# Performance work log

Measured on AMD Instinct MI355X. Metric: run time of the kernel, lower is better.

Reference implementation:

```python
import jax, jax.numpy as jnp
import numpy as np
import math

B, S, D, M, H = 4, 2048, 1024, 512, 8
DK = M // H


def setup_inputs() -> dict:
    key = jax.random.key(0)
    ks = jax.random.split(key, 16)
    sd = lambda fan_in: 1.0 / math.sqrt(fan_in)
    inp = {
        'x': jax.random.normal(ks[0], (B, S, D), dtype=jnp.float32),
        'W_enc': jax.random.normal(ks[1], (D, M), dtype=jnp.float32) * sd(D),
        'b_enc': jnp.zeros((M,), jnp.float32),
        'Wq': jax.random.normal(ks[2], (M, M), dtype=jnp.float32) * sd(M),
        'bq': jnp.zeros((M,), jnp.float32),
        'Wk': jax.random.normal(ks[3], (M, M), dtype=jnp.float32) * sd(M),
        'bk': jnp.zeros((M,), jnp.float32),
        'Wv': jax.random.normal(ks[4], (M, M), dtype=jnp.float32) * sd(M),
        'bv': jnp.zeros((M,), jnp.float32),
        'Wo': jax.random.normal(ks[5], (M, M), dtype=jnp.float32) * sd(M),
        'bo': jnp.zeros((M,), jnp.float32),
        'ocr_bias': jnp.zeros((1, H, 1, 1), jnp.float32),  # learned, init zeros
        'W1': jax.random.normal(ks[6], (D + M, D), dtype=jnp.float32) * sd(D + M),
        'b1': jnp.zeros((D,), jnp.float32),
        'W2': jax.random.normal(ks[7], (D, D), dtype=jnp.float32) * sd(D),
        'b2': jnp.zeros((D,), jnp.float32),
        'ln_g': jnp.ones((D,), jnp.float32),
        'ln_b': jnp.zeros((D,), jnp.float32),
    }
    return inp


def _ocr_attention(m, Wq, bq, Wk, bk, Wv, bv, Wo, bo, ocr_bias):
    b, s, _ = m.shape
    q = (m @ Wq + bq).reshape(b, s, H, DK).transpose(0, 2, 1, 3)  # bhsd
    k = (m @ Wk + bk).reshape(b, s, H, DK).transpose(0, 2, 1, 3)
    v = (m @ Wv + bv).reshape(b, s, H, DK).transpose(0, 2, 1, 3)
    scores = jnp.einsum('bhqd,bhkd->bhqk', q, k) / math.sqrt(DK) + ocr_bias
    attn = jax.nn.softmax(scores, axis=-1)  # dropout is identity at eval
    ctx = jnp.einsum('bhqk,bhkd->bhqd', attn, v)
    ctx = ctx.transpose(0, 2, 1, 3).reshape(b, s, M)
    return ctx @ Wo + bo


def _layernorm(h, g, bta, eps=1e-5):
    mu = jnp.mean(h, axis=-1, keepdims=True)
    var = jnp.mean(jnp.square(h - mu), axis=-1, keepdims=True)
    return (h - mu) * jax.lax.rsqrt(var + eps) * g + bta


def reference(x, W_enc, b_enc, Wq, bq, Wk, bk, Wv, bv, Wo, bo, ocr_bias, W1, b1, W2, b2, ln_g, ln_b):
    mem = x @ W_enc + b_enc  # [B,S,M] memory-dim stream
    attended = _ocr_attention(mem, Wq, bq, Wk, bk, Wv, bv, Wo, bo, ocr_bias)
    h = jnp.concatenate([x, attended], axis=-1) @ W1 + b1  # [B,S,D]
    h = jax.nn.gelu(h, approximate=False)
    h = h @ W2 + b2
    return _layernorm(h, ln_g, ln_b)
```

## Files before the change

### kernel.cpp

```cpp
#include <hip/hip_runtime.h>
#include <math.h>

#define B_ 4
#define S_ 2048
#define D_ 1024
#define M_ 512
#define H_ 8
#define R_ (B_ * S_)

typedef __bf16 bf8_t __attribute__((ext_vector_type(8)));
typedef __bf16 bf4_t __attribute__((ext_vector_type(4)));
typedef float f4_t __attribute__((ext_vector_type(4)));

typedef __attribute__((address_space(3))) void lds_void;
typedef const __attribute__((address_space(1))) void gl_void;
#define GL16(gp, lp) __builtin_amdgcn_global_load_lds((gl_void*)(gp), (lds_void*)(lp), 16, 0, 0)

__device__ inline unsigned packbf2(float a, float b) {
  union { __bf16 h[2]; unsigned u; } c;
  c.h[0] = (__bf16)a;
  c.h[1] = (__bf16)b;
  return c.u;
}
__device__ inline unsigned bperm(int srcBytes, unsigned v) {
  return (unsigned)__builtin_amdgcn_ds_bpermute(srcBytes, (int)v);
}

struct PrepArgs {
  const float* src[7];
  __bf16* dst[7];
  int K[7], N[7];
  int start[8];
  const float* x;
  __bf16* ab;
};

__global__ __launch_bounds__(256) void k_prep(PrepArgs a) {
  const int t = threadIdx.x;
  const int id = blockIdx.x;
  if (id < a.start[7]) {
    int w = 0;
    while (id >= a.start[w + 1]) ++w;
    const int local = id - a.start[w];
    const int bxw = a.N[w] >> 5;
    const int n0 = (local % bxw) * 32;
    const int k0 = (local / bxw) * 32;
    const int tx = t & 31, ty = t >> 5;
    __shared__ float tile[32][33];
    const float* in = a.src[w];
    __bf16* out = a.dst[w];
    const int N = a.N[w], K = a.K[w];
#pragma unroll
    for (int j = 0; j < 32; j += 8)
      tile[ty + j][tx] = in[(size_t)(k0 + ty + j) * N + n0 + tx];
    __syncthreads();
#pragma unroll
    for (int j = 0; j < 32; j += 8)
      out[(size_t)(n0 + ty + j) * K + k0 + tx] = (__bf16)tile[tx][ty + j];
  } else {
    size_t i = (((size_t)(id - a.start[7])) * 256 + t) * 8;
    size_t row = i >> 10;
    size_t col = i & 1023;
    f4_t f0 = *(const f4_t*)(a.x + i);
    f4_t f1 = *(const f4_t*)(a.x + i + 4);
    bf8_t v;
    v[0] = (__bf16)f0[0]; v[1] = (__bf16)f0[1]; v[2] = (__bf16)f0[2]; v[3] = (__bf16)f0[3];
    v[4] = (__bf16)f1[0]; v[5] = (__bf16)f1[1]; v[6] = (__bf16)f1[2]; v[7] = (__bf16)f1[3];
    *(bf8_t*)(a.ab + row * 1536 + col) = v;
  }
}

template <int EPI>
__global__ __launch_bounds__(256) void k_gemm_bt(const __bf16* __restrict__ A, int lda,
                                                 const __bf16* __restrict__ Bt,
                                                 const float* __restrict__ bias,
                                                 __bf16* __restrict__ C, int ldc, int K) {
  __shared__ __bf16 As[128 * 32];
  __shared__ __bf16 Bs[128 * 32];
  const int t = threadIdx.x;
  const int lane = t & 63;
  const int wv = t >> 6;
  const int wr = (wv >> 1) * 64;
  const int wc = (wv & 1) * 64;
  const int bm = blockIdx.y * 128;
  const int bn = blockIdx.x * 128;
  const int c0 = wv * 2, c1 = wv * 2 + 1;
  const int sr0 = c0 * 16 + (lane >> 2);
  const int sr1 = c1 * 16 + (lane >> 2);
  const int scol = (lane & 3) * 8;
  const __bf16* Ag0 = A + (size_t)(bm + sr0) * lda + scol;
  const __bf16* Ag1 = A + (size_t)(bm + sr1) * lda + scol;
  const __bf16* Bg0 = Bt + (size_t)(bn + sr0) * (size_t)K + scol;
  const __bf16* Bg1 = Bt + (size_t)(bn + sr1) * (size_t)K + scol;
  __bf16* Al0 = As + c0 * 512;
  __bf16* Al1 = As + c1 * 512;
  __bf16* Bl0 = Bs + c0 * 512;
  __bf16* Bl1 = Bs + c1 * 512;
  f4_t acc[4][4];
#pragma unroll
  for (int m = 0; m < 4; ++m)
#pragma unroll
    for (int n = 0; n < 4; ++n) acc[m][n] = (f4_t){0.f, 0.f, 0.f, 0.f};
  const int fr = lane & 15;
  const int fk = (lane >> 4) * 8;
  for (int k0 = 0; k0 < K; k0 += 32) {
    __syncthreads();
    GL16(Ag0 + k0, Al0);
    GL16(Ag1 + k0, Al1);
    GL16(Bg0 + k0, Bl0);
    GL16(Bg1 + k0, Bl1);
    __syncthreads();
    bf8_t af[4], bfr[4];
#pragma unroll
    for (int m = 0; m < 4; ++m) af[m] = *(const bf8_t*)&As[(wr + m * 16 + fr) * 32 + fk];
#pragma unroll
    for (int n = 0; n < 4; ++n) bfr[n] = *(const bf8_t*)&Bs[(wc + n * 16 + fr) * 32 + fk];
#pragma unroll
    for (int m = 0; m < 4; ++m)
#pragma unroll
      for (int n = 0; n < 4; ++n)
        acc[m][n] = __builtin_amdgcn_mfma_f32_16x16x32_bf16(af[m], bfr[n], acc[m][n], 0, 0, 0);
  }
  const int cr = (lane >> 4) * 4;
  const int cc = lane & 15;
#pragma unroll
  for (int n = 0; n < 4; ++n) {
    const int col = bn + wc + n * 16 + cc;
    const float bv = bias[col];
#pragma unroll
    for (int m = 0; m < 4; ++m)
#pragma unroll
      for (int r = 0; r < 4; ++r) {
        const int row = bm + wr + m * 16 + cr + r;
        float v = acc[m][n][r] + bv;
        if (EPI == 1) v = 0.5f * v * (1.0f + erff(v * 0.70710678118f));
        C[(size_t)row * ldc + col] = (__bf16)v;
      }
  }
}

__global__ __launch_bounds__(256) void k_gemm_qkv(const __bf16* __restrict__ A,
                                                  const __bf16* __restrict__ Bt,
                                                  const float* __restrict__ bq,
                                                  const float* __restrict__ bk,
                                                  const float* __restrict__ bvb,
                                                  __bf16* __restrict__ qb,
                                                  __bf16* __restrict__ pkd,
                                                  __bf16* __restrict__ pvd) {
  const int K = 512;
  __shared__ __bf16 As[128 * 32];
  __shared__ __bf16 Bs[128 * 32];
  const int t = threadIdx.x;
  const int lane = t & 63;
  const int wv = t >> 6;
  const int wr = (wv >> 1) * 64;
  const int wc = (wv & 1) * 64;
  const int bm = blockIdx.y * 128;
  const int bn = blockIdx.x * 128;
  const int c0 = wv * 2, c1 = wv * 2 + 1;
  const int sr0 = c0 * 16 + (lane >> 2);
  const int sr1 = c1 * 16 + (lane >> 2);
  const int scol = (lane & 3) * 8;
  const __bf16* Ag0 = A + (size_t)(bm + sr0) * K + scol;
  const __bf16* Ag1 = A + (size_t)(bm + sr1) * K + scol;
  const __bf16* Bg0 = Bt + (size_t)(bn + sr0) * (size_t)K + scol;
  const __bf16* Bg1 = Bt + (size_t)(bn + sr1) * (size_t)K + scol;
  __bf16* Al0 = As + c0 * 512;
  __bf16* Al1 = As + c1 * 512;
  __bf16* Bl0 = Bs + c0 * 512;
  __bf16* Bl1 = Bs + c1 * 512;
  f4_t acc[4][4];
#pragma unroll
  for (int m = 0; m < 4; ++m)
#pragma unroll
    for (int n = 0; n < 4; ++n) acc[m][n] = (f4_t){0.f, 0.f, 0.f, 0.f};
  const int fr = lane & 15;
  const int fk = (lane >> 4) * 8;
  for (int k0 = 0; k0 < K; k0 += 32) {
    __syncthreads();
    GL16(Ag0 + k0, Al0);
    GL16(Ag1 + k0, Al1);
    GL16(Bg0 + k0, Bl0);
    GL16(Bg1 + k0, Bl1);
    __syncthreads();
    bf8_t af[4], bfr[4];
#pragma unroll
    for (int m = 0; m < 4; ++m) af[m] = *(const bf8_t*)&As[(wr + m * 16 + fr) * 32 + fk];
#pragma unroll
    for (int n = 0; n < 4; ++n) bfr[n] = *(const bf8_t*)&Bs[(wc + n * 16 + fr) * 32 + fk];
#pragma unroll
    for (int m = 0; m < 4; ++m)
#pragma unroll
      for (int n = 0; n < 4; ++n)
        acc[m][n] = __builtin_amdgcn_mfma_f32_16x16x32_bf16(af[m], bfr[n], acc[m][n], 0, 0, 0);
  }
  const int cr = (lane >> 4) * 4;
  const int cc = lane & 15;
  const int seg = bn >> 9;
  const int b0 = bm >> 11;
  if (seg == 0) {
#pragma unroll
    for (int n = 0; n < 4; ++n) {
      const int col = (bn + wc + n * 16 + cc) & 511;
      const float bvv = bq[col];
#pragma unroll
      for (int m = 0; m < 4; ++m)
#pragma unroll
        for (int r = 0; r < 4; ++r) {
          const int row = bm + wr + m * 16 + cr + r;
          qb[(size_t)row * 512 + col] = (__bf16)(acc[m][n][r] + bvv);
        }
    }
  } else if (seg == 1) {
#pragma unroll
    for (int n = 0; n < 4; ++n) {
      const int col = (bn + wc + n * 16 + cc) & 511;
      const int hh = col >> 6, d = col & 63;
      const int s = d >> 5, g2 = (d >> 3) & 3, e = d & 7;
      const float bvv = bk[col];
#pragma unroll
      for (int m = 0; m < 4; ++m)
#pragma unroll
        for (int r = 0; r < 4; ++r) {
          const int key = (bm + wr + m * 16 + cr + r) & 2047;
          const int k16 = key >> 4, frk = key & 15;
          pkd[(((size_t)(b0 * 8 + hh) * 128 + k16) * 2 + s) * 512 + (g2 * 16 + frk) * 8 + e] =
              (__bf16)(acc[m][n][r] + bvv);
        }
    }
  } else {
#pragma unroll
    for (int n = 0; n < 4; ++n) {
      const int col = (bn + wc + n * 16 + cc) & 511;
      const int hh = col >> 6, dd = col & 63;
      const int d16 = dd >> 4, fv = dd & 15;
      const float bvv = bvb[col];
#pragma unroll
      for (int m = 0; m < 4; ++m) {
        const int keyb = (bm + wr + m * 16 + cr) & 2047;
        const int kc = keyb >> 6, ks = (keyb >> 5) & 1, g2 = (keyb >> 3) & 3, e0 = keyb & 7;
        bf4_t w;
#pragma unroll
        for (int r = 0; r < 4; ++r) w[r] = (__bf16)(acc[m][n][r] + bvv);
        *(bf4_t*)&pvd[((((size_t)(b0 * 8 + hh) * 32 + kc) * 2 + ks) * 4 + d16) * 512 +
                      (g2 * 16 + fv) * 8 + e0] = w;
      }
    }
  }
}

__global__ __launch_bounds__(256, 2) void k_attn4(const __bf16* __restrict__ qb,
                                                  const __bf16* __restrict__ pk,
                                                  const __bf16* __restrict__ pv,
                                                  __bf16* __restrict__ ctx) {
  __shared__ __bf16 KL[8192];
  __shared__ __bf16 VL[8192];
  const int t = threadIdx.x;
  const int lane = t & 63;
  const int wv = t >> 6;
  const int i = blockIdx.x;
  const int xcd = i & 7;
  const int jj = i >> 3;
  const int bh = xcd + 8 * (jj & 3);
  const int xt = jj >> 2;
  const int b = bh >> 3, h = bh & 7;
  const int q0 = xt * 128 + wv * 32;
  const int fr = lane & 15;
  const int g = lane >> 4;
  const int fk = g * 8;
  const float qs = 0.125f * 1.44269504f;
  bf8_t bqf[2][2];
#pragma unroll
  for (int tt = 0; tt < 2; ++tt)
#pragma unroll
    for (int s = 0; s < 2; ++s) {
      bf8_t raw = *(const bf8_t*)(qb + ((size_t)b * S_ + q0 + tt * 16 + fr) * M_ + h * 64 + s * 32 + fk);
      bf8_t sc;
#pragma unroll
      for (int e = 0; e < 8; ++e) sc[e] = (__bf16)((float)raw[e] * qs);
      bqf[tt][s] = sc;
    }
  const __bf16* pkc = pk + (size_t)bh * 131072;
  const __bf16* pvc = pv + (size_t)bh * 131072;
  float mreg[2] = {-3e38f, -3e38f};
  float lreg[2] = {0.f, 0.f};
  f4_t o[2][4];
#pragma unroll
  for (int tt = 0; tt < 2; ++tt)
#pragma unroll
    for (int d = 0; d < 4; ++d) o[tt][d] = (f4_t){0.f, 0.f, 0.f, 0.f};
  const int srcA = (fr + ((g & 1) << 5)) << 2;
  const int srcB = srcA + 64;

#define STAGE(KV)                                                                      \
  {                                                                                    \
    const size_t goff = (size_t)(KV) * 64;                                             \
    _Pragma("unroll") for (int j = 0; j < 4; ++j) {                                    \
      GL16(pkc + goff + (wv * 4 + j) * 512 + lane * 8, KL + (wv * 4 + j) * 512);       \
      GL16(pvc + goff + (wv * 4 + j) * 512 + lane * 8, VL + (wv * 4 + j) * 512);       \
    }                                                                                  \
  }

#define COMPUTE64(HALF)                                                                   \
  {                                                                                       \
    bf8_t ak[4][2], bvf[2][4];                                                            \
    _Pragma("unroll") for (int hh = 0; hh < 4; ++hh)                                      \
        _Pragma("unroll") for (int s = 0; s < 2; ++s)                                     \
            ak[hh][s] = *(const bf8_t*)&KL[(HALF) * 4096 + (hh * 2 + s) * 512 + lane * 8];\
    _Pragma("unroll") for (int ks = 0; ks < 2; ++ks)                                      \
        _Pragma("unroll") for (int d = 0; d < 4; ++d)                                     \
            bvf[ks][d] = *(const bf8_t*)&VL[(HALF) * 4096 + (ks * 4 + d) * 512 + lane * 8];\
    f4_t st[2][4];                                                                        \
    __builtin_amdgcn_s_setprio(1);                                                        \
    _Pragma("unroll") for (int tt = 0; tt < 2; ++tt)                                      \
        _Pragma("unroll") for (int hh = 0; hh < 4; ++hh) {                                \
      f4_t a = (f4_t){0.f, 0.f, 0.f, 0.f};                                                \
      a = __builtin_amdgcn_mfma_f32_16x16x32_bf16(ak[hh][0], bqf[tt][0], a, 0, 0, 0);     \
      a = __builtin_amdgcn_mfma_f32_16x16x32_bf16(ak[hh][1], bqf[tt][1], a, 0, 0, 0);     \
      st[tt][hh] = a;                                                                     \
    }                                                                                     \
    __builtin_amdgcn_s_setprio(0);                                                        \
    _Pragma("unroll") for (int tt = 0; tt < 2; ++tt) {                                    \
      float pm = -3e38f;                                                                  \
      _Pragma("unroll") for (int hh = 0; hh < 4; ++hh)                                    \
          _Pragma("unroll") for (int r = 0; r < 4; ++r) pm = fmaxf(pm, st[tt][hh][r]);    \
      pm = fmaxf(pm, __shfl_xor(pm, 16, 64));                                             \
      pm = fmaxf(pm, __shfl_xor(pm, 32, 64));                                             \
      float mo = mreg[tt];                                                                \
      if (!__all(pm <= mo + 8.f)) {                                                       \
        const float mn = fmaxf(mo, pm);                                                   \
        const float al = exp2f(mo - mn);                                                  \
        mreg[tt] = mn;                                                                    \
        mo = mn;                                                                          \
        lreg[tt] *= al;                                                                   \
        float alr[4];                                                                     \
        _Pragma("unroll") for (int r = 0; r < 4; ++r) alr[r] = __shfl(al, g * 4 + r, 64); \
        _Pragma("unroll") for (int d = 0; d < 4; ++d)                                     \
            _Pragma("unroll") for (int r = 0; r < 4; ++r) o[tt][d][r] *= alr[r];          \
      }                                                                                   \
      float p[4][4];                                                                      \
      float ps = 0.f;                                                                     \
      _Pragma("unroll") for (int hh = 0; hh < 4; ++hh)                                    \
          _Pragma("unroll") for (int r = 0; r < 4; ++r) {                                 \
        p[hh][r] = exp2f(st[tt][hh][r] - mo);                                             \
        ps += p[hh][r];                                                                   \
      }                                                                                   \
      ps += __shfl_xor(ps, 16, 64);                                                       \
      ps += __shfl_xor(ps, 32, 64);                                                       \
      lreg[tt] += ps;                                                                     \
      union { unsigned u[4]; bf8_t v; } aw[2];                                            \
      _Pragma("unroll") for (int ks = 0; ks < 2; ++ks) {                                  \
        unsigned ch0 = packbf2(p[2 * ks][0], p[2 * ks][1]);                               \
        unsigned ch1 = packbf2(p[2 * ks][2], p[2 * ks][3]);                               \
        unsigned ch2 = packbf2(p[2 * ks + 1][0], p[2 * ks + 1][1]);                       \
        unsigned ch3 = packbf2(p[2 * ks + 1][2], p[2 * ks + 1][3]);                       \
        unsigned t0 = bperm(srcA, ch0), t2 = bperm(srcA, ch2);                            \
        unsigned t1 = bperm(srcA, ch1), t3 = bperm(srcA, ch3);                            \
        unsigned u0 = bperm(srcB, ch0), u2 = bperm(srcB, ch2);                            \
        unsigned u1 = bperm(srcB, ch1), u3 = bperm(srcB, ch3);                            \
        const bool lo = (g < 2);                                                          \
        aw[ks].u[0] = lo ? t0 : t2;                                                       \
        aw[ks].u[1] = lo ? t1 : t3;                                                       \
        aw[ks].u[2] = lo ? u0 : u2;                                                       \
        aw[ks].u[3] = lo ? u1 : u3;                                                       \
      }                                                                                   \
      __builtin_amdgcn_s_setprio(1);                                                      \
      _Pragma("unroll") for (int d = 0; d < 4; ++d) {                                     \
        o[tt][d] = __builtin_amdgcn_mfma_f32_16x16x32_bf16(aw[0].v, bvf[0][d], o[tt][d], 0, 0, 0); \
        o[tt][d] = __builtin_amdgcn_mfma_f32_16x16x32_bf16(aw[1].v, bvf[1][d], o[tt][d], 0, 0, 0); \
      }                                                                                   \
      __builtin_amdgcn_s_setprio(0);                                                      \
    }                                                                                     \
  }

  STAGE(0);
  for (int kv = 0; kv < S_; kv += 128) {
    __syncthreads();
    COMPUTE64(0);
    COMPUTE64(1);
    __syncthreads();
    if (kv + 128 < S_) STAGE(kv + 128);
  }
#undef STAGE
#undef COMPUTE64

#pragma unroll
  for (int tt = 0; tt < 2; ++tt) {
    float lrr[4];
#pragma unroll
    for (int r = 0; r < 4; ++r) lrr[r] = __shfl(lreg[tt], g * 4 + r, 64);
#pragma unroll
    for (int d = 0; d < 4; ++d)
#pragma unroll
      for (int r = 0; r < 4; ++r) {
        const float v = o[tt][d][r] / lrr[r];
        ctx[((size_t)b * S_ + q0 + tt * 16 + g * 4 + r) * M_ + h * 64 + d * 16 + fr] = (__bf16)v;
      }
  }
}

__global__ __launch_bounds__(256) void k_ln(const __bf16* __restrict__ hh,
                                            const float* __restrict__ g,
                                            const float* __restrict__ bt,
                                            float* __restrict__ out) {
  const int row = blockIdx.x;
  const int t = threadIdx.x;
  const __bf16* hp = hh + (size_t)row * 1024 + t * 4;
  bf4_t v = *(const bf4_t*)hp;
  float f[4];
  float s1 = 0.f, s2 = 0.f;
#pragma unroll
  for (int j = 0; j < 4; ++j) {
    f[j] = (float)v[j];
    s1 += f[j];
    s2 += f[j] * f[j];
  }
#pragma unroll
  for (int d = 1; d < 64; d <<= 1) {
    s1 += __shfl_xor(s1, d, 64);
    s2 += __shfl_xor(s2, d, 64);
  }
  __shared__ float red[8];
  const int lane = t & 63, wv = t >> 6;
  if (lane == 0) { red[wv] = s1; red[4 + wv] = s2; }
  __syncthreads();
  const float S1 = red[0] + red[1] + red[2] + red[3];
  const float S2 = red[4] + red[5] + red[6] + red[7];
  const float mu = S1 * (1.f / 1024.f);
  const float var = S2 * (1.f / 1024.f) - mu * mu;
  const float inv = rsqrtf(var + 1e-5f);
  float* op = out + (size_t)row * 1024 + t * 4;
#pragma unroll
  for (int j = 0; j < 4; ++j) op[j] = (f[j] - mu) * inv * g[t * 4 + j] + bt[t * 4 + j];
}

extern "C" void kernel_launch(void* const* d_in, const int* in_sizes, int n_in,
                              void* d_out, int out_size, void* d_ws, size_t ws_size,
                              hipStream_t stream) {
  const float* x = (const float*)d_in[0];
  const float* W_enc = (const float*)d_in[1];
  const float* b_enc = (const float*)d_in[2];
  const float* Wq = (const float*)d_in[3];
  const float* bq = (const float*)d_in[4];
  const float* Wk = (const float*)d_in[5];
  const float* bk = (const float*)d_in[6];
  const float* Wv = (const float*)d_in[7];
  const float* bv = (const float*)d_in[8];
  const float* Wo = (const float*)d_in[9];
  const float* bo = (const float*)d_in[10];
  const float* W1 = (const float*)d_in[12];
  const float* b1 = (const float*)d_in[13];
  const float* W2 = (const float*)d_in[14];
  const float* b2 = (const float*)d_in[15];
  const float* lng = (const float*)d_in[16];
  const float* lnb = (const float*)d_in[17];
  float* out = (float*)d_out;

  __bf16* p = (__bf16*)d_ws;
  __bf16* ab = p;  p += (size_t)R_ * 1536;
  __bf16* mem = p; p += (size_t)R_ * 512;
  __bf16* qb = p;  p += (size_t)R_ * 512;
  __bf16* pk = p;  p += (size_t)R_ * 512;
  __bf16* pv = p;  p += (size_t)R_ * 512;
  __bf16* cx = p;  p += (size_t)R_ * 512;
  __bf16* h1 = p;  p += (size_t)R_ * 1024;
  __bf16* h2 = p;  p += (size_t)R_ * 1024;
  __bf16* WtE = p; p += (size_t)512 * 1024;
  __bf16* WtQ = p; p += (size_t)512 * 512;
  __bf16* WtK = p; p += (size_t)512 * 512;
  __bf16* WtV = p; p += (size_t)512 * 512;
  __bf16* WtO = p; p += (size_t)512 * 512;
  __bf16* Wt1 = p; p += (size_t)1024 * 1536;
  __bf16* Wt2 = p; p += (size_t)1024 * 1024;

  PrepArgs pa;
  pa.src[0] = W_enc; pa.dst[0] = WtE; pa.K[0] = 1024; pa.N[0] = 512;
  pa.src[1] = Wq;    pa.dst[1] = WtQ; pa.K[1] = 512;  pa.N[1] = 512;
  pa.src[2] = Wk;    pa.dst[2] = WtK; pa.K[2] = 512;  pa.N[2] = 512;
  pa.src[3] = Wv;    pa.dst[3] = WtV; pa.K[3] = 512;  pa.N[3] = 512;
  pa.src[4] = Wo;    pa.dst[4] = WtO; pa.K[4] = 512;  pa.N[4] = 512;
  pa.src[5] = W1;    pa.dst[5] = Wt1; pa.K[5] = 1536; pa.N[5] = 1024;
  pa.src[6] = W2;    pa.dst[6] = Wt2; pa.K[6] = 1024; pa.N[6] = 1024;
  int acc0 = 0;
  for (int w = 0; w < 7; ++w) {
    pa.start[w] = acc0;
    acc0 += (pa.N[w] >> 5) * (pa.K[w] >> 5);
  }
  pa.start[7] = acc0;
  pa.x = x; pa.ab = ab;
  k_prep<<<acc0 + 4096, 256, 0, stream>>>(pa);
  k_gemm_bt<0><<<dim3(4, 64), 256, 0, stream>>>(ab, 1536, WtE, b_enc, mem, 512, 1024);
  k_gemm_qkv<<<dim3(12, 64), 256, 0, stream>>>(mem, WtQ, bq, bk, bv, qb, pk, pv);
  k_attn4<<<512, 256, 0, stream>>>(qb, pk, pv, cx);
  k_gemm_bt<0><<<dim3(4, 64), 256, 0, stream>>>(cx, 512, WtO, bo, ab + 1024, 1536, 512);
  k_gemm_bt<1><<<dim3(8, 64), 256, 0, stream>>>(ab, 1536, Wt1, b1, h1, 1024, 1536);
  k_gemm_bt<0><<<dim3(8, 64), 256, 0, stream>>>(h1, 1024, Wt2, b2, h2, 1024, 1024);
  k_ln<<<R_, 256, 0, stream>>>(h2, lng, lnb, out);
}
```

Measured before the change: 370.1 us.

## Double-buffer LDS in GEMMs and attention, shrink tiles for more blocks

Converts the GEMM, QKV GEMM and attention kernels to double-buffered LDS staging, so the next K/KV tile is prefetched while MFMAs run on the current one, with a single barrier per iteration. Adds a templated BM so the narrow N=512 GEMMs use 64-row tiles and launch twice as many blocks. The attention kernel handles 16 queries per wave instead of 32, uses 64-key chunks, launches 1024 blocks and requests occupancy 4. The aim is to hide global-load latency and fill more CUs, at the cost of more LDS per block and less reuse of each K/V tile.

Result: faster. 360.4 us (-2.6%).

```diff
diff --git a/kernel.cpp b/kernel.cpp
--- a/kernel.cpp
+++ b/kernel.cpp
@@ -70,57 +70,62 @@
   }
 }
 
-template <int EPI>
-__global__ __launch_bounds__(256) void k_gemm_bt(const __bf16* __restrict__ A, int lda,
-                                                 const __bf16* __restrict__ Bt,
-                                                 const float* __restrict__ bias,
-                                                 __bf16* __restrict__ C, int ldc, int K) {
-  __shared__ __bf16 As[128 * 32];
-  __shared__ __bf16 Bs[128 * 32];
+template <int BM, int EPI>
+__global__ __launch_bounds__(256) void k_gemm2(const __bf16* __restrict__ A, int lda,
+                                               const __bf16* __restrict__ Bt,
+                                               const float* __restrict__ bias,
+                                               __bf16* __restrict__ C, int ldc, int K) {
+  constexpr int ACH = BM / 16;
+  constexpr int MR = BM / 32;
+  __shared__ __bf16 As[2][BM * 32];
+  __shared__ __bf16 Bs[2][128 * 32];
   const int t = threadIdx.x;
   const int lane = t & 63;
   const int wv = t >> 6;
-  const int wr = (wv >> 1) * 64;
+  const int wr = (wv >> 1) * (BM / 2);
   const int wc = (wv & 1) * 64;
-  const int bm = blockIdx.y * 128;
+  const int bm = blockIdx.y * BM;
   const int bn = blockIdx.x * 128;
-  const int c0 = wv * 2, c1 = wv * 2 + 1;
-  const int sr0 = c0 * 16 + (lane >> 2);
-  const int sr1 = c1 * 16 + (lane >> 2);
+  const int srow = lane >> 2;
   const int scol = (lane & 3) * 8;
-  const __bf16* Ag0 = A + (size_t)(bm + sr0) * lda + scol;
-  const __bf16* Ag1 = A + (size_t)(bm + sr1) * lda + scol;
-  const __bf16* Bg0 = Bt + (size_t)(bn + sr0) * (size_t)K + scol;
-  const __bf16* Bg1 = Bt + (size_t)(bn + sr1) * (size_t)K + scol;
-  __bf16* Al0 = As + c0 * 512;
-  __bf16* Al1 = As + c1 * 512;
-  __bf16* Bl0 = Bs + c0 * 512;
-  __bf16* Bl1 = Bs + c1 * 512;
-  f4_t acc[4][4];
-#pragma unroll
-  for (int m = 0; m < 4; ++m)
+  f4_t acc[MR][4];
+#pragma unroll
+  for (int m = 0; m < MR; ++m)
 #pragma unroll
     for (int n = 0; n < 4; ++n) acc[m][n] = (f4_t){0.f, 0.f, 0.f, 0.f};
   const int fr = lane & 15;
   const int fk = (lane >> 4) * 8;
-  for (int k0 = 0; k0 < K; k0 += 32) {
-    __syncthreads();
-    GL16(Ag0 + k0, Al0);
-    GL16(Ag1 + k0, Al1);
-    GL16(Bg0 + k0, Bl0);
-    GL16(Bg1 + k0, Bl1);
-    __syncthreads();
-    bf8_t af[4], bfr[4];
-#pragma unroll
-    for (int m = 0; m < 4; ++m) af[m] = *(const bf8_t*)&As[(wr + m * 16 + fr) * 32 + fk];
-#pragma unroll
-    for (int n = 0; n < 4; ++n) bfr[n] = *(const bf8_t*)&Bs[(wc + n * 16 + fr) * 32 + fk];
-#pragma unroll
-    for (int m = 0; m < 4; ++m)
+  const int NT = K >> 5;
+
+#define STAGE_G(k0, buf)                                                                   \
+  {                                                                                        \
+    _Pragma("unroll") for (int c = wv; c < ACH; c += 4)                                    \
+        GL16(A + (size_t)(bm + c * 16 + srow) * lda + (k0) + scol, &As[buf][c * 512]);     \
+    _Pragma("unroll") for (int c = wv; c < 8; c += 4)                                      \
+        GL16(Bt + (size_t)(bn + c * 16 + srow) * (size_t)K + (k0) + scol, &Bs[buf][c * 512]); \
+  }
+
+  STAGE_G(0, 0);
+  __syncthreads();
+  for (int it = 0; it < NT; ++it) {
+    const int cur = it & 1;
+    if (it + 1 < NT) STAGE_G((it + 1) << 5, cur ^ 1);
+    bf8_t af[MR], bfr[4];
+#pragma unroll
+    for (int m = 0; m < MR; ++m) af[m] = *(const bf8_t*)&As[cur][(wr + m * 16 + fr) * 32 + fk];
+#pragma unroll
+    for (int n = 0; n < 4; ++n) bfr[n] = *(const bf8_t*)&Bs[cur][(wc + n * 16 + fr) * 32 + fk];
+    __builtin_amdgcn_s_setprio(1);
+#pragma unroll
+    for (int m = 0; m < MR; ++m)
 #pragma unroll
       for (int n = 0; n < 4; ++n)
         acc[m][n] = __builtin_amdgcn_mfma_f32_16x16x32_bf16(af[m], bfr[n], acc[m][n], 0, 0, 0);
-  }
+    __builtin_amdgcn_s_setprio(0);
+    __syncthreads();
+  }
+#undef STAGE_G
+
   const int cr = (lane >> 4) * 4;
   const int cc = lane & 15;
 #pragma unroll
@@ -128,7 +133,7 @@
     const int col = bn + wc + n * 16 + cc;
     const float bv = bias[col];
 #pragma unroll
-    for (int m = 0; m < 4; ++m)
+    for (int m = 0; m < MR; ++m)
 #pragma unroll
       for (int r = 0; r < 4; ++r) {
         const int row = bm + wr + m * 16 + cr + r;
@@ -148,8 +153,8 @@
                                                   __bf16* __restrict__ pkd,
                                                   __bf16* __restrict__ pvd) {
   const int K = 512;
-  __shared__ __bf16 As[128 * 32];
-  __shared__ __bf16 Bs[128 * 32];
+  __shared__ __bf16 As[2][128 * 32];
+  __shared__ __bf16 Bs[2][128 * 32];
   const int t = threadIdx.x;
   const int lane = t & 63;
   const int wv = t >> 6;
@@ -157,18 +162,8 @@
   const int wc = (wv & 1) * 64;
   const int bm = blockIdx.y * 128;
   const int bn = blockIdx.x * 128;
-  const int c0 = wv * 2, c1 = wv * 2 + 1;
-  const int sr0 = c0 * 16 + (lane >> 2);
-  const int sr1 = c1 * 16 + (lane >> 2);
+  const int srow = lane >> 2;
   const int scol = (lane & 3) * 8;
-  const __bf16* Ag0 = A + (size_t)(bm + sr0) * K + scol;
-  const __bf16* Ag1 = A + (size_t)(bm + sr1) * K + scol;
-  const __bf16* Bg0 = Bt + (size_t)(bn + sr0) * (size_t)K + scol;
-  const __bf16* Bg1 = Bt + (size_t)(bn + sr1) * (size_t)K + scol;
-  __bf16* Al0 = As + c0 * 512;
-  __bf16* Al1 = As + c1 * 512;
-  __bf16* Bl0 = Bs + c0 * 512;
-  __bf16* Bl1 = Bs + c1 * 512;
   f4_t acc[4][4];
 #pragma unroll
   for (int m = 0; m < 4; ++m)
@@ -176,24 +171,36 @@
     for (int n = 0; n < 4; ++n) acc[m][n] = (f4_t){0.f, 0.f, 0.f, 0.f};
   const int fr = lane & 15;
   const int fk = (lane >> 4) * 8;
-  for (int k0 = 0; k0 < K; k0 += 32) {
-    __syncthreads();
-    GL16(Ag0 + k0, Al0);
-    GL16(Ag1 + k0, Al1);
-    GL16(Bg0 + k0, Bl0);
-    GL16(Bg1 + k0, Bl1);
-    __syncthreads();
+
+#define STAGE_Q(k0, buf)                                                                   \
+  {                                                                                        \
+    _Pragma("unroll") for (int c = wv; c < 8; c += 4) {                                    \
+      GL16(A + (size_t)(bm + c * 16 + srow) * K + (k0) + scol, &As[buf][c * 512]);         \
+      GL16(Bt + (size_t)(bn + c * 16 + srow) * (size_t)K + (k0) + scol, &Bs[buf][c * 512]); \
+    }                                                                                      \
+  }
+
+  STAGE_Q(0, 0);
+  __syncthreads();
+  for (int it = 0; it < 16; ++it) {
+    const int cur = it & 1;
+    if (it + 1 < 16) STAGE_Q((it + 1) << 5, cur ^ 1);
     bf8_t af[4], bfr[4];
 #pragma unroll
-    for (int m = 0; m < 4; ++m) af[m] = *(const bf8_t*)&As[(wr + m * 16 + fr) * 32 + fk];
-#pragma unroll
-    for (int n = 0; n < 4; ++n) bfr[n] = *(const bf8_t*)&Bs[(wc + n * 16 + fr) * 32 + fk];
+    for (int m = 0; m < 4; ++m) af[m] = *(const bf8_t*)&As[cur][(wr + m * 16 + fr) * 32 + fk];
+#pragma unroll
+    for (int n = 0; n < 4; ++n) bfr[n] = *(const bf8_t*)&Bs[cur][(wc + n * 16 + fr) * 32 + fk];
+    __builtin_amdgcn_s_setprio(1);
 #pragma unroll
     for (int m = 0; m < 4; ++m)
 #pragma unroll
       for (int n = 0; n < 4; ++n)
         acc[m][n] = __builtin_amdgcn_mfma_f32_16x16x32_bf16(af[m], bfr[n], acc[m][n], 0, 0, 0);
-  }
+    __builtin_amdgcn_s_setprio(0);
+    __syncthreads();
+  }
+#undef STAGE_Q
+
   const int cr = (lane >> 4) * 4;
   const int cc = lane & 15;
   const int seg = bn >> 9;
@@ -249,12 +256,12 @@
   }
 }
 
-__global__ __launch_bounds__(256, 2) void k_attn4(const __bf16* __restrict__ qb,
+__global__ __launch_bounds__(256, 4) void k_attn5(const __bf16* __restrict__ qb,
                                                   const __bf16* __restrict__ pk,
                                                   const __bf16* __restrict__ pv,
                                                   __bf16* __restrict__ ctx) {
-  __shared__ __bf16 KL[8192];
-  __shared__ __bf16 VL[8192];
+  __shared__ __bf16 KL[2][4096];
+  __shared__ __bf16 VL[2][4096];
   const int t = threadIdx.x;
   const int lane = t & 63;
   const int wv = t >> 6;
@@ -262,141 +269,139 @@
   const int xcd = i & 7;
   const int jj = i >> 3;
   const int bh = xcd + 8 * (jj & 3);
-  const int xt = jj >> 2;
+  const int qt = jj >> 2;
   const int b = bh >> 3, h = bh & 7;
-  const int q0 = xt * 128 + wv * 32;
+  const int q0 = qt * 64 + wv * 16;
   const int fr = lane & 15;
   const int g = lane >> 4;
   const int fk = g * 8;
   const float qs = 0.125f * 1.44269504f;
-  bf8_t bqf[2][2];
-#pragma unroll
-  for (int tt = 0; tt < 2; ++tt)
-#pragma unroll
-    for (int s = 0; s < 2; ++s) {
-      bf8_t raw = *(const bf8_t*)(qb + ((size_t)b * S_ + q0 + tt * 16 + fr) * M_ + h * 64 + s * 32 + fk);
-      bf8_t sc;
-#pragma unroll
-      for (int e = 0; e < 8; ++e) sc[e] = (__bf16)((float)raw[e] * qs);
-      bqf[tt][s] = sc;
-    }
+  bf8_t bqf[2];
+#pragma unroll
+  for (int s = 0; s < 2; ++s) {
+    bf8_t raw = *(const bf8_t*)(qb + ((size_t)b * S_ + q0 + fr) * M_ + h * 64 + s * 32 + fk);
+    bf8_t sc;
+#pragma unroll
+    for (int e = 0; e < 8; ++e) sc[e] = (__bf16)((float)raw[e] * qs);
+    bqf[s] = sc;
+  }
   const __bf16* pkc = pk + (size_t)bh * 131072;
   const __bf16* pvc = pv + (size_t)bh * 131072;
-  float mreg[2] = {-3e38f, -3e38f};
-  float lreg[2] = {0.f, 0.f};
-  f4_t o[2][4];
-#pragma unroll
-  for (int tt = 0; tt < 2; ++tt)
-#pragma unroll
-    for (int d = 0; d < 4; ++d) o[tt][d] = (f4_t){0.f, 0.f, 0.f, 0.f};
+  float mreg = -3e38f, lreg = 0.f;
+  f4_t o[4];
+#pragma unroll
+  for (int d = 0; d < 4; ++d) o[d] = (f4_t){0.f, 0.f, 0.f, 0.f};
   const int srcA = (fr + ((g & 1) << 5)) << 2;
   const int srcB = srcA + 64;
 
-#define STAGE(KV)                                                                      \
-  {                                                                                    \
-    const size_t goff = (size_t)(KV) * 64;                                             \
-    _Pragma("unroll") for (int j = 0; j < 4; ++j) {                                    \
-      GL16(pkc + goff + (wv * 4 + j) * 512 + lane * 8, KL + (wv * 4 + j) * 512);       \
-      GL16(pvc + goff + (wv * 4 + j) * 512 + lane * 8, VL + (wv * 4 + j) * 512);       \
-    }                                                                                  \
-  }
-
-#define COMPUTE64(HALF)                                                                   \
-  {                                                                                       \
-    bf8_t ak[4][2], bvf[2][4];                                                            \
-    _Pragma("unroll") for (int hh = 0; hh < 4; ++hh)                                      \
-        _Pragma("unroll") for (int s = 0; s < 2; ++s)                                     \
-            ak[hh][s] = *(const bf8_t*)&KL[(HALF) * 4096 + (hh * 2 + s) * 512 + lane * 8];\
-    _Pragma("unroll") for (int ks = 0; ks < 2; ++ks)                                      \
-        _Pragma("unroll") for (int d = 0; d < 4; ++d)                                     \
-            bvf[ks][d] = *(const bf8_t*)&VL[(HALF) * 4096 + (ks * 4 + d) * 512 + lane * 8];\
-    f4_t st[2][4];                                                                        \
-    __builtin_amdgcn_s_setprio(1);                                                        \
-    _Pragma("unroll") for (int tt = 0; tt < 2; ++tt)                                      \
-        _Pragma("unroll") for (int hh = 0; hh < 4; ++hh) {                                \
-      f4_t a = (f4_t){0.f, 0.f, 0.f, 0.f};                                                \
-      a = __builtin_amdgcn_mfma_f32_16x16x32_bf16(ak[hh][0], bqf[tt][0], a, 0, 0, 0);     \
-      a = __builtin_amdgcn_mfma_f32_16x16x32_bf16(ak[hh][1], bqf[tt][1], a, 0, 0, 0);     \
-      st[tt][hh] = a;                                                                     \
-    }                                                                                     \
-    __builtin_amdgcn_s_setprio(0);                                                        \
-    _Pragma("unroll") for (int tt = 0; tt < 2; ++tt) {                                    \
-      float pm = -3e38f;                                                                  \
-      _Pragma("unroll") for (int hh = 0; hh < 4; ++hh)                                    \
-          _Pragma("unroll") for (int r = 0; r < 4; ++r) pm = fmaxf(pm, st[tt][hh][r]);    \
-      pm = fmaxf(pm, __shfl_xor(pm, 16, 64));                                             \
-      pm = fmaxf(pm, __shfl_xor(pm, 32, 64));                                             \
-      float mo = mreg[tt];                                                                \
-      if (!__all(pm <= mo + 8.f)) {                                                       \
-        const float mn = fmaxf(mo, pm);                                                   \
-        const float al = exp2f(mo - mn);                                                  \
-        mreg[tt] = mn;                                                                    \
-        mo = mn;                                                                          \
-        lreg[tt] *= al;                                                                   \
-        float alr[4];                                                                     \
-        _Pragma("unroll") for (int r = 0; r < 4; ++r) alr[r] = __shfl(al, g * 4 + r, 64); \
-        _Pragma("unroll") for (int d = 0; d < 4; ++d)                                     \
-            _Pragma("unroll") for (int r = 0; r < 4; ++r) o[tt][d][r] *= alr[r];          \
-      }                                                                                   \
-      float p[4][4];                                                                      \
-      float ps = 0.f;                                                                     \
-      _Pragma("unroll") for (int hh = 0; hh < 4; ++hh)                                    \
-          _Pragma("unroll") for (int r = 0; r < 4; ++r) {                                 \
-        p[hh][r] = exp2f(st[tt][hh][r] - mo);                                             \
-        ps += p[hh][r];                                                                   \
-      }                                                                                   \
-      ps += __shfl_xor(ps, 16, 64);                                                       \
-      ps += __shfl_xor(ps, 32, 64);                                                       \
-      lreg[tt] += ps;                                                                     \
-      union { unsigned u[4]; bf8_t v; } aw[2];                                            \
-      _Pragma("unroll") for (int ks = 0; ks < 2; ++ks) {                                  \
-        unsigned ch0 = packbf2(p[2 * ks][0], p[2 * ks][1]);                               \
-        unsigned ch1 = packbf2(p[2 * ks][2], p[2 * ks][3]);                               \
-        unsigned ch2 = packbf2(p[2 * ks + 1][0], p[2 * ks + 1][1]);                       \
-        unsigned ch3 = packbf2(p[2 * ks + 1][2], p[2 * ks + 1][3]);                       \
-        unsigned t0 = bperm(srcA, ch0), t2 = bperm(srcA, ch2);                            \
-        unsigned t1 = bperm(srcA, ch1), t3 = bperm(srcA, ch3);                            \
-        unsigned u0 = bperm(srcB, ch0), u2 = bperm(srcB, ch2);                            \
-        unsigned u1 = bperm(srcB, ch1), u3 = bperm(srcB, ch3);                            \
-        const bool lo = (g < 2);                                                          \
-        aw[ks].u[0] = lo ? t0 : t2;                                                       \
-        aw[ks].u[1] = lo ? t1 : t3;                                                       \
-        aw[ks].u[2] = lo ? u0 : u2;                                                       \
-        aw[ks].u[3] = lo ? u1 : u3;                                                       \
-      }                                                                                   \
-      __builtin_amdgcn_s_setprio(1);                                                      \
-      _Pragma("unroll") for (int d = 0; d < 4; ++d) {                                     \
-        o[tt][d] = __builtin_amdgcn_mfma_f32_16x16x32_bf16(aw[0].v, bvf[0][d], o[tt][d], 0, 0, 0); \
-        o[tt][d] = __builtin_amdgcn_mfma_f32_16x16x32_bf16(aw[1].v, bvf[1][d], o[tt][d], 0, 0, 0); \
-      }                                                                                   \
-      __builtin_amdgcn_s_setprio(0);                                                      \
-    }                                                                                     \
-  }
-
-  STAGE(0);
-  for (int kv = 0; kv < S_; kv += 128) {
+#define STAGEA(c, buf)                                                      \
+  {                                                                         \
+    const __bf16* kg = pkc + (size_t)(c) * 4096;                            \
+    const __bf16* vg = pvc + (size_t)(c) * 4096;                            \
+    GL16(kg + (wv * 2 + 0) * 512 + lane * 8, &KL[buf][(wv * 2 + 0) * 512]); \
+    GL16(kg + (wv * 2 + 1) * 512 + lane * 8, &KL[buf][(wv * 2 + 1) * 512]); \
+    GL16(vg + (wv * 2 + 0) * 512 + lane * 8, &VL[buf][(wv * 2 + 0) * 512]); \
+    GL16(vg + (wv * 2 + 1) * 512 + lane * 8, &VL[buf][(wv * 2 + 1) * 512]); \
+  }
+
+  STAGEA(0, 0);
+  __syncthreads();
+  for (int c = 0; c < 32; ++c) {
+    const int cur = c & 1;
+    if (c + 1 < 32) STAGEA(c + 1, cur ^ 1);
+    bf8_t ak[4][2], bvf[2][4];
+#pragma unroll
+    for (int hh = 0; hh < 4; ++hh)
+#pragma unroll
+      for (int s = 0; s < 2; ++s)
+        ak[hh][s] = *(const bf8_t*)&KL[cur][(hh * 2 + s) * 512 + lane * 8];
+#pragma unroll
+    for (int ks = 0; ks < 2; ++ks)
+#pragma unroll
+      for (int d = 0; d < 4; ++d)
+        bvf[ks][d] = *(const bf8_t*)&VL[cur][(ks * 4 + d) * 512 + lane * 8];
+    f4_t st[4];
+    __builtin_amdgcn_s_setprio(1);
+#pragma unroll
+    for (int hh = 0; hh < 4; ++hh) {
+      f4_t a = (f4_t){0.f, 0.f, 0.f, 0.f};
+      a = __builtin_amdgcn_mfma_f32_16x16x32_bf16(ak[hh][0], bqf[0], a, 0, 0, 0);
+      a = __builtin_amdgcn_mfma_f32_16x16x32_bf16(ak[hh][1], bqf[1], a, 0, 0, 0);
+      st[hh] = a;
+    }
+    __builtin_amdgcn_s_setprio(0);
+    float pm = -3e38f;
+#pragma unroll
+    for (int hh = 0; hh < 4; ++hh)
+#pragma unroll
+      for (int r = 0; r < 4; ++r) pm = fmaxf(pm, st[hh][r]);
+    pm = fmaxf(pm, __shfl_xor(pm, 16, 64));
+    pm = fmaxf(pm, __shfl_xor(pm, 32, 64));
+    float mo = mreg;
+    if (!__all(pm <= mo + 8.f)) {
+      const float mn = fmaxf(mo, pm);
+      const float al = exp2f(mo - mn);
+      mreg = mn;
+      mo = mn;
+      lreg *= al;
+      float alr[4];
+#pragma unroll
+      for (int r = 0; r < 4; ++r) alr[r] = __shfl(al, g * 4 + r, 64);
+#pragma unroll
+      for (int d = 0; d < 4; ++d)
+#pragma unroll
+        for (int r = 0; r < 4; ++r) o[d][r] *= alr[r];
+    }
+    float p[4][4];
+    float ps = 0.f;
+#pragma unroll
+    for (int hh = 0; hh < 4; ++hh)
+#pragma unroll
+      for (int r = 0; r < 4; ++r) {
+        p[hh][r] = exp2f(st[hh][r] - mo);
+        ps += p[hh][r];
+      }
+    ps += __shfl_xor(ps, 16, 64);
+    ps += __shfl_xor(ps, 32, 64);
+    lreg += ps;
+    union { unsigned u[4]; bf8_t v; } aw[2];
+#pragma unroll
+    for (int ks = 0; ks < 2; ++ks) {
+      unsigned ch0 = packbf2(p[2 * ks][0], p[2 * ks][1]);
+      unsigned ch1 = packbf2(p[2 * ks][2], p[2 * ks][3]);
+      unsigned ch2 = packbf2(p[2 * ks + 1][0], p[2 * ks + 1][1]);
+      unsigned ch3 = packbf2(p[2 * ks + 1][2], p[2 * ks + 1][3]);
+      unsigned t0 = bperm(srcA, ch0), t2 = bperm(srcA, ch2);
+      unsigned t1 = bperm(srcA, ch1), t3 = bperm(srcA, ch3);
+      unsigned u0 = bperm(srcB, ch0), u2 = bperm(srcB, ch2);
+      unsigned u1 = bperm(srcB, ch1), u3 = bperm(srcB, ch3);
+      const bool lo = (g < 2);
+      aw[ks].u[0] = lo ? t0 : t2;
+      aw[ks].u[1] = lo ? t1 : t3;
+      aw[ks].u[2] = lo ? u0 : u2;
+      aw[ks].u[3] = lo ? u1 : u3;
+    }
+    __builtin_amdgcn_s_setprio(1);
+#pragma unroll
+    for (int d = 0; d < 4; ++d) {
+      o[d] = __builtin_amdgcn_mfma_f32_16x16x32_bf16(aw[0].v, bvf[0][d], o[d], 0, 0, 0);
+      o[d] = __builtin_amdgcn_mfma_f32_16x16x32_bf16(aw[1].v, bvf[1][d], o[d], 0, 0, 0);
+    }
+    __builtin_amdgcn_s_setprio(0);
     __syncthreads();
-    COMPUTE64(0);
-    COMPUTE64(1);
-    __syncthreads();
-    if (kv + 128 < S_) STAGE(kv + 128);
-  }
-#undef STAGE
-#undef COMPUTE64
-
-#pragma unroll
-  for (int tt = 0; tt < 2; ++tt) {
-    float lrr[4];
-#pragma unroll
-    for (int r = 0; r < 4; ++r) lrr[r] = __shfl(lreg[tt], g * 4 + r, 64);
-#pragma unroll
-    for (int d = 0; d < 4; ++d)
-#pragma unroll
-      for (int r = 0; r < 4; ++r) {
-        const float v = o[tt][d][r] / lrr[r];
-        ctx[((size_t)b * S_ + q0 + tt * 16 + g * 4 + r) * M_ + h * 64 + d * 16 + fr] = (__bf16)v;
-      }
-  }
+  }
+#undef STAGEA
+
+  float lrr[4];
+#pragma unroll
+  for (int r = 0; r < 4; ++r) lrr[r] = __shfl(lreg, g * 4 + r, 64);
+#pragma unroll
+  for (int d = 0; d < 4; ++d)
+#pragma unroll
+    for (int r = 0; r < 4; ++r) {
+      const float v = o[d][r] / lrr[r];
+      ctx[((size_t)b * S_ + q0 + g * 4 + r) * M_ + h * 64 + d * 16 + fr] = (__bf16)v;
+    }
 }
 
 __global__ __launch_bounds__(256) void k_ln(const __bf16* __restrict__ hh,
@@ -489,11 +494,11 @@
   pa.start[7] = acc0;
   pa.x = x; pa.ab = ab;
   k_prep<<<acc0 + 4096, 256, 0, stream>>>(pa);
-  k_gemm_bt<0><<<dim3(4, 64), 256, 0, stream>>>(ab, 1536, WtE, b_enc, mem, 512, 1024);
+  k_gemm2<64, 0><<<dim3(4, 128), 256, 0, stream>>>(ab, 1536, WtE, b_enc, mem, 512, 1024);
   k_gemm_qkv<<<dim3(12, 64), 256, 0, stream>>>(mem, WtQ, bq, bk, bv, qb, pk, pv);
-  k_attn4<<<512, 256, 0, stream>>>(qb, pk, pv, cx);
-  k_gemm_bt<0><<<dim3(4, 64), 256, 0, stream>>>(cx, 512, WtO, bo, ab + 1024, 1536, 512);
-  k_gemm_bt<1><<<dim3(8, 64), 256, 0, stream>>>(ab, 1536, Wt1, b1, h1, 1024, 1536);
-  k_gemm_bt<0><<<dim3(8, 64), 256, 0, stream>>>(h1, 1024, Wt2, b2, h2, 1024, 1024);
+  k_attn5<<<1024, 256, 0, stream>>>(qb, pk, pv, cx);
+  k_gemm2<64, 0><<<dim3(4, 128), 256, 0, stream>>>(cx, 512, WtO, bo, ab + 1024, 1536, 512);
+  k_gemm2<128, 1><<<dim3(8, 64), 256, 0, stream>>>(ab, 1536, Wt1, b1, h1, 1024, 1536);
+  k_gemm2<128, 0><<<dim3(8, 64), 256, 0, stream>>>(h1, 1024, Wt2, b2, h2, 1024, 1024);
   k_ln<<<R_, 256, 0, stream>>>(h2, lng, lnb, out);
 }
```
